# Kernel optimization log

Measured on AMD Instinct MI355X. Metric: run time of the kernel, lower is better.

Reference implementation:

```python
import jax, jax.numpy as jnp
import numpy as np

# Architecture constants (from init_kwargs / mamba_ssm Mamba2 defaults)
D_MODEL = 256
D_STATE = 64
D_CONV = 4
EXPAND = 2
HEADDIM = 64
D_INNER = EXPAND * D_MODEL          # 512
NHEADS = D_INNER // HEADDIM         # 8
CONV_DIM = D_INNER + 2 * D_STATE    # 640 (ngroups=1)
D_IN_PROJ = 2 * D_INNER + 2 * D_STATE + NHEADS  # 1160
NUM_LAYERS = 4
EPS = 1e-5


def _mamba2_block(h, ipw, cw, cb, dtb, alog, dpar, rmsw, opw):
    # h: (b, l, d_model)
    b, l, _ = h.shape
    zxbcdt = h @ ipw                                  # (b, l, D_IN_PROJ)
    z = zxbcdt[..., :D_INNER]
    xBC = zxbcdt[..., D_INNER:D_INNER + CONV_DIM]
    dt = zxbcdt[..., -NHEADS:]

    # causal depthwise conv1d over the sequence, then SiLU
    xBC = jnp.swapaxes(xBC, 1, 2)                     # (b, CONV_DIM, l)
    xBC = jax.lax.conv_general_dilated(
        xBC, cw[:, None, :], (1,), [(D_CONV - 1, 0)],
        feature_group_count=CONV_DIM)
    xBC = jax.nn.silu(xBC + cb[None, :, None])
    xBC = jnp.swapaxes(xBC, 1, 2)                     # (b, l, CONV_DIM)

    xh = xBC[..., :D_INNER].reshape(b, l, NHEADS, HEADDIM)
    Bm = xBC[..., D_INNER:D_INNER + D_STATE]          # (b, l, n)
    Cm = xBC[..., D_INNER + D_STATE:]                 # (b, l, n)

    dt = jax.nn.softplus(dt + dtb)                    # (b, l, h)
    A = -jnp.exp(alog)                                # (h,)

    def step(state, ins):
        # state: (b, h, p, n)
        x_t, dt_t, B_t, C_t = ins                     # (b,h,p),(b,h),(b,n),(b,n)
        dA = jnp.exp(dt_t * A)                        # (b, h)
        state = state * dA[:, :, None, None] + jnp.einsum('bh,bhp,bn->bhpn', dt_t, x_t, B_t)
        y = jnp.einsum('bhpn,bn->bhp', state, C_t)
        return state, y

    xs = (jnp.swapaxes(xh, 0, 1), jnp.swapaxes(dt, 0, 1),
          jnp.swapaxes(Bm, 0, 1), jnp.swapaxes(Cm, 0, 1))
    init = jnp.zeros((b, NHEADS, HEADDIM, D_STATE), h.dtype)
    _, ys = jax.lax.scan(step, init, xs)              # ys: (l, b, h, p)
    y = jnp.swapaxes(ys, 0, 1) + dpar[None, None, :, None] * xh
    y = y.reshape(b, l, D_INNER)

    # gated RMSNorm (norm(y * silu(z)) * weight), then out projection
    y = y * jax.nn.silu(z)
    y = y * jax.lax.rsqrt(jnp.mean(y * y, -1, keepdims=True) + EPS) * rmsw
    return y @ opw


def setup_inputs() -> dict:
    key = jax.random.key(0)
    ks = jax.random.split(key, 12)
    B, L, F = 16, 2048, 46
    inp = {
        'x': jax.random.normal(ks[0], (B, L, F), jnp.float32),
        'inp_w': jax.random.normal(ks[1], (F, D_MODEL), jnp.float32) * 0.1,
        'inp_b': jnp.zeros((D_MODEL,), jnp.float32),
        'in_proj_w': jax.random.normal(ks[2], (NUM_LAYERS, D_MODEL, D_IN_PROJ), jnp.float32) * 0.02,
        'conv_w': jax.random.normal(ks[3], (NUM_LAYERS, CONV_DIM, D_CONV), jnp.float32) * 0.2,
        'conv_b': jnp.zeros((NUM_LAYERS, CONV_DIM), jnp.float32),
        'dt_bias': jax.random.normal(ks[4], (NUM_LAYERS, NHEADS), jnp.float32) * 0.5,
        'A_log': jnp.log(jax.random.uniform(ks[5], (NUM_LAYERS, NHEADS), jnp.float32, 1.0, 16.0)),
        'D': jnp.ones((NUM_LAYERS, NHEADS), jnp.float32),
        'rms_w': jnp.ones((NUM_LAYERS, D_INNER), jnp.float32),
        'out_proj_w': jax.random.normal(ks[6], (NUM_LAYERS, D_INNER, D_MODEL), jnp.float32) * 0.02,
        'ln_w': jnp.ones((D_MODEL,), jnp.float32),
        'ln_b': jnp.zeros((D_MODEL,), jnp.float32),
        'dir_w': jax.random.normal(ks[7], (D_MODEL, 1), jnp.float32) * 0.05,
        'dir_b': jnp.zeros((1,), jnp.float32),
        'reg_w': jax.random.normal(ks[8], (D_MODEL, 3), jnp.float32) * 0.05,
        'reg_b': jnp.zeros((3,), jnp.float32),
    }
    return inp


def reference(x, inp_w, inp_b, in_proj_w, conv_w, conv_b, dt_bias, A_log, D,
              rms_w, out_proj_w, ln_w, ln_b, dir_w, dir_b, reg_w, reg_b):
    h = x @ inp_w + inp_b
    for i in range(NUM_LAYERS):
        h = h + _mamba2_block(h, in_proj_w[i], conv_w[i], conv_b[i], dt_bias[i],
                              A_log[i], D[i], rms_w[i], out_proj_w[i])
    mu = jnp.mean(h, -1, keepdims=True)
    var = jnp.mean((h - mu) ** 2, -1, keepdims=True)
    h = (h - mu) * jax.lax.rsqrt(var + EPS) * ln_w + ln_b
    h = jnp.mean(h, axis=1)                           # mean-pool over sequence
    # dropout is identity in eval mode
    dir_logits = h @ dir_w + dir_b
    reg_out = h @ reg_w + reg_b
    return (dir_logits, reg_out)
```

## Files before the change

kernel.cpp:

```cpp
#include <hip/hip_runtime.h>
#include <hip/hip_bf16.h>
#include <math.h>

typedef __hip_bfloat16 bf16;

#define B_ 16
#define L_ 2048
#define DM 256
#define DI 512
#define NH 8
#define HD 64
#define DS 64
#define CD 640
#define DIP 1160
#define XB 648
#define NP 1280
#define NL 4
#define Q_ 64
#define NCH 32
#define MROWS (B_*L_)
#define EPS_ 1e-5f
#define NIN 17
#define NSMALL 14
#define STGOFF 32
#define WIPT 28552
#define WOPT 683912
#define HMPOFF 946056
#define SLICEOFF 1011592
#define PERROW 2004

__device__ __forceinline__ float u2f(unsigned short u){ return __uint_as_float(((unsigned)u)<<16); }
__device__ __forceinline__ unsigned short f2bu(float f){ bf16 h = __float2bfloat16(f); return *(unsigned short*)&h; }
__device__ __forceinline__ float sigmoidf_(float x){ return 1.f/(1.f+__expf(-x)); }
__device__ __forceinline__ float siluf_(float x){ return x*sigmoidf_(x); }
__device__ __forceinline__ float softplusf_(float x){ return (x>20.f)? x : log1pf(__expf(x)); }

typedef __attribute__((ext_vector_type(8))) short short8v;
typedef __attribute__((ext_vector_type(4))) float float4v;
typedef __attribute__((ext_vector_type(8))) unsigned short ush8;

__device__ const int kN17[NIN] = {1507328,11776,256,1187840,10240,2560,32,32,32,2048,524288,256,256,256,1,768,3};
__device__ const int sIdx[NSMALL] = {1,2,4,5,6,7,8,9,11,12,13,14,15,16};
__device__ const int sNum[NSMALL] = {11776,256,10240,2560,32,32,32,2048,256,256,256,1,768,3};
__device__ const int sOff[NSMALL] = {0,11776,12032,22272,24832,24864,24896,24928,26976,27232,27488,27744,27748,28516};

struct PtrTab { const void* p[NIN]; };

__global__ __launch_bounds__(64) void k_sentinel(float* out, float v){
    int t = threadIdx.x;
    out[t] = (t==0) ? v : 0.f;
}

__global__ __launch_bounds__(256) void k_detect(PtrTab t, int* flags){
    int i = blockIdx.x;
    int n = kN17[i];
    int S = n < 4096 ? n : 4096;
    const unsigned short* u = (const unsigned short*)t.p[i];
    __shared__ int big, ze, zo, so;
    if (threadIdx.x == 0){ big=0; ze=0; zo=0; so=0; }
    __syncthreads();
    int lbig=0, lze=0, lzo=0, lso=0;
    for (int j=threadIdx.x; j<S; j+=256){
        unsigned short v = u[j];
        int e = (v>>7)&0xFF;
        if (e >= 131) lbig = 1;
        int isz = ((v & 0x7FFF) == 0) ? 1 : 0;
        if (j & 1){ lso++; lzo += isz; } else { lze += isz; }
    }
    if (lbig) atomicOr(&big, 1);
    atomicAdd(&ze, lze); atomicAdd(&zo, lzo); atomicAdd(&so, lso);
    __syncthreads();
    if (threadIdx.x == 0){
        int Se = S - so;
        flags[i] = (big || (so > 0 && 4*ze >= 3*Se && 4*zo <= so)) ? 1 : 0;
    }
}

__global__ __launch_bounds__(256) void k_stage(PtrTab t, const int* __restrict__ flags,
                                               float* __restrict__ stg){
    int a = blockIdx.y;
    int idx = sIdx[a];
    int n = sNum[a];
    float* dst = stg + sOff[a];
    const void* p = t.p[idx];
    if (flags[idx]){
        const float* s = (const float*)p;
        for (int j=blockIdx.x*256+threadIdx.x; j<n; j += gridDim.x*256) dst[j] = s[j];
    } else {
        const unsigned short* s = (const unsigned short*)p;
        for (int j=blockIdx.x*256+threadIdx.x; j<n; j += gridDim.x*256) dst[j] = u2f(s[j]);
    }
}

__global__ __launch_bounds__(256) void k_wip(const void* __restrict__ src,
                                             const int* __restrict__ flag,
                                             unsigned short* __restrict__ dst){
    int n = blockIdx.x, l = blockIdx.y, k = threadIdx.x;
    unsigned short b = 0;
    if (n < DIP){
        size_t si = ((size_t)l*DM + k)*DIP + n;
        if (flag[0]) b = f2bu(((const float*)src)[si]);
        else         b = ((const unsigned short*)src)[si];
    }
    dst[((size_t)l*NP + n)*DM + k] = b;
}

__global__ __launch_bounds__(256) void k_wop(const void* __restrict__ src,
                                             const int* __restrict__ flag,
                                             unsigned short* __restrict__ dst){
    int n = blockIdx.x, l = blockIdx.y;
    for (int k = threadIdx.x; k < DI; k += 256){
        size_t si = ((size_t)l*DI + k)*DM + n;
        unsigned short b;
        if (flag[0]) b = f2bu(((const float*)src)[si]);
        else         b = ((const unsigned short*)src)[si];
        dst[((size_t)l*DM + n)*DI + k] = b;
    }
}

__device__ __forceinline__ float blockSum256(float v, float* red){
    #pragma unroll
    for (int off=32; off>0; off>>=1) v += __shfl_down(v, off);
    if ((threadIdx.x & 63) == 0) red[threadIdx.x >> 6] = v;
    __syncthreads();
    float s = red[0] + red[1] + red[2] + red[3];
    __syncthreads();
    return s;
}

__global__ __launch_bounds__(256) void k_inproj(const void* __restrict__ x,
                                                const int* __restrict__ flags,
                                                size_t xoff,
                                                const float* __restrict__ w,
                                                const float* __restrict__ bias,
                                                float* __restrict__ h,
                                                unsigned short* __restrict__ hbf){
    __shared__ float xs[32*46];
    int row0 = blockIdx.x*32;
    int t = threadIdx.x;
    bool f32 = flags[0] != 0;
    for (int j = t; j < 32*46; j += 256){
        size_t gi = xoff + (size_t)row0*46 + j;
        xs[j] = f32 ? ((const float*)x)[gi] : u2f(((const unsigned short*)x)[gi]);
    }
    __syncthreads();
    float bv = bias[t];
    float acc[32];
    #pragma unroll
    for (int r=0;r<32;r++) acc[r] = bv;
    for (int k=0;k<46;k++){
        float wv = w[k*DM + t];
        #pragma unroll
        for (int r=0;r<32;r++) acc[r] += xs[r*46 + k]*wv;
    }
    #pragma unroll
    for (int r=0;r<32;r++){
        size_t o = (size_t)(row0 + r)*DM + t;
        h[o] = acc[r];
        hbf[o] = f2bu(acc[r]);
    }
}

template<int MODE>
__global__ __launch_bounds__(256, 4) void k_mgemm(const unsigned short* __restrict__ A,
                                                  const unsigned short* __restrict__ Bt,
                                                  float* __restrict__ O1,
                                                  unsigned short* __restrict__ O1b,
                                                  unsigned short* __restrict__ O2b,
                                                  unsigned short* __restrict__ O3,
                                                  int K){
    __shared__ __align__(16) char ldsraw[16896];
    unsigned short* As = (unsigned short*)ldsraw;
    unsigned short* Bs = (unsigned short*)(ldsraw + 5120);
    int tid = threadIdx.x;
    int wave = tid >> 6, lane = tid & 63, quad = lane >> 4, l15 = lane & 15;
    int p = blockIdx.y * gridDim.x + blockIdx.x;
    int nwg = gridDim.x * gridDim.y;
    int cpx = nwg >> 3;
    int logical = (p & 7) * cpx + (p >> 3);
    int by = logical / gridDim.x;
    int bx = logical - by * gridDim.x;
    int mbase = by*64, nbase = bx*128;
    int wm = (wave & 1)*32, wn = (wave >> 1)*64;
    float4v zero4 = {0.f,0.f,0.f,0.f};
    float4v acc[2][4];
    #pragma unroll
    for (int mi=0;mi<2;mi++)
        #pragma unroll
        for (int ni=0;ni<4;ni++) acc[mi][ni] = zero4;

    int rowA = tid >> 2, koffA = (tid & 3)*8;
    const unsigned short* Ap = A + (size_t)(mbase+rowA)*K + koffA;
    for (int k0 = 0; k0 < K; k0 += 32){
        *(uint4*)&As[rowA*40 + koffA] = *(const uint4*)&Ap[k0];
        #pragma unroll
        for (int i=0;i<2;i++){
            int c = tid + i*256;
            int row = c >> 2, koff = (c & 3)*8;
            *(uint4*)&Bs[row*40 + koff] = *(const uint4*)&Bt[(size_t)(nbase+row)*K + k0 + koff];
        }
        __syncthreads();
        short8v af[2], bfr[4];
        #pragma unroll
        for (int mi=0;mi<2;mi++) af[mi] = *(const short8v*)&As[(wm + mi*16 + l15)*40 + quad*8];
        #pragma unroll
        for (int ni=0;ni<4;ni++) bfr[ni] = *(const short8v*)&Bs[(wn + ni*16 + l15)*40 + quad*8];
        #pragma unroll
        for (int mi=0;mi<2;mi++)
            #pragma unroll
            for (int ni=0;ni<4;ni++)
                acc[mi][ni] = __builtin_amdgcn_mfma_f32_16x16x32_bf16(af[mi], bfr[ni], acc[mi][ni], 0, 0, 0);
        __syncthreads();
    }

    float* ep = (float*)ldsraw;
    int erow = tid >> 4;
    int ecc  = (tid & 15) * 8;
    #pragma unroll
    for (int half = 0; half < 2; ++half){
        if ((wave & 1) == half){
            #pragma unroll
            for (int mi=0;mi<2;mi++){
                #pragma unroll
                for (int ni=0;ni<4;ni++){
                    int col = wn + ni*16 + l15;
                    #pragma unroll
                    for (int reg=0;reg<4;reg++){
                        int r = mi*16 + quad*4 + reg;
                        ep[r*132 + col] = acc[mi][ni][reg];
                    }
                }
            }
        }
        __syncthreads();
        #pragma unroll
        for (int ps=0; ps<2; ps++){
            int r = ps*16 + erow;
            int growg = mbase + half*32 + r;
            int colg = nbase + ecc;
            float4 v0 = *(const float4*)&ep[r*132 + ecc + 0];
            float4 v1 = *(const float4*)&ep[r*132 + ecc + 4];
            if (MODE == 0){
                ush8 ob;
                ob[0]=f2bu(v0.x); ob[1]=f2bu(v0.y); ob[2]=f2bu(v0.z); ob[3]=f2bu(v0.w);
                ob[4]=f2bu(v1.x); ob[5]=f2bu(v1.y); ob[6]=f2bu(v1.z); ob[7]=f2bu(v1.w);
                if (colg + 8 <= DI){
                    *(ush8*)&O1b[(size_t)growg*DI + colg] = ob;
                } else if (colg >= DI && colg + 8 <= DIP){
                    *(ush8*)&O2b[(size_t)growg*XB + (colg - DI)] = ob;
                }
            } else {
                size_t ob1 = (size_t)growg*DM + colg;
                float4 h0 = *(const float4*)&O1[ob1];
                float4 h1 = *(const float4*)&O1[ob1+4];
                h0.x+=v0.x; h0.y+=v0.y; h0.z+=v0.z; h0.w+=v0.w;
                h1.x+=v1.x; h1.y+=v1.y; h1.z+=v1.z; h1.w+=v1.w;
                *(float4*)&O1[ob1] = h0;
                *(float4*)&O1[ob1+4] = h1;
                ush8 ob;
                ob[0]=f2bu(h0.x); ob[1]=f2bu(h0.y); ob[2]=f2bu(h0.z); ob[3]=f2bu(h0.w);
                ob[4]=f2bu(h1.x); ob[5]=f2bu(h1.y); ob[6]=f2bu(h1.z); ob[7]=f2bu(h1.w);
                *(ush8*)&O3[ob1] = ob;
            }
        }
        __syncthreads();
    }
}

__global__ __launch_bounds__(256) void k_conv(const unsigned short* __restrict__ xbb,
                                              const float* __restrict__ cw,
                                              const float* __restrict__ cb,
                                              unsigned short* __restrict__ cvb){
    int tid = threadIdx.x;
    int c0 = (blockIdx.x*16 + (tid & 15))*4;
    int r0 = blockIdx.y*64 + (tid >> 4);
    float wA[4], wB[4], wC[4], wD[4];
    {
        float4 t0 = *(const float4*)&cw[(size_t)(c0+0)*4];
        float4 t1 = *(const float4*)&cw[(size_t)(c0+1)*4];
        float4 t2 = *(const float4*)&cw[(size_t)(c0+2)*4];
        float4 t3 = *(const float4*)&cw[(size_t)(c0+3)*4];
        wA[0]=t0.x; wA[1]=t0.y; wA[2]=t0.z; wA[3]=t0.w;
        wB[0]=t1.x; wB[1]=t1.y; wB[2]=t1.z; wB[3]=t1.w;
        wC[0]=t2.x; wC[1]=t2.y; wC[2]=t2.z; wC[3]=t2.w;
        wD[0]=t3.x; wD[1]=t3.y; wD[2]=t3.z; wD[3]=t3.w;
    }
    float4 bb = *(const float4*)&cb[c0];
    #pragma unroll
    for (int i=0;i<4;i++){
        int r = r0 + i*16;
        int l = r & (L_-1);
        float a0=bb.x, a1=bb.y, a2=bb.z, a3=bb.w;
        #pragma unroll
        for (int j=0;j<4;j++){
            if (l-3+j >= 0){
                ushort4 uv = *(const ushort4*)&xbb[(size_t)(r-3+j)*XB + c0];
                a0 += u2f(uv.x)*wA[j];
                a1 += u2f(uv.y)*wB[j];
                a2 += u2f(uv.z)*wC[j];
                a3 += u2f(uv.w)*wD[j];
            }
        }
        ushort4 ov;
        ov.x = f2bu(siluf_(a0));
        ov.y = f2bu(siluf_(a1));
        ov.z = f2bu(siluf_(a2));
        ov.w = f2bu(siluf_(a3));
        *(ushort4*)&cvb[(size_t)r*CD + c0] = ov;
    }
}

__global__ __launch_bounds__(64) void k_dtcum(const unsigned short* __restrict__ xb,
                                              const float* __restrict__ dtb,
                                              const float* __restrict__ alog,
                                              float* __restrict__ dto,
                                              float* __restrict__ cumo){
    int kk = blockIdx.x, h = blockIdx.y, b = blockIdx.z;
    int t = threadIdx.x;
    int l = kk*Q_ + t;
    float raw = u2f(xb[(size_t)(b*L_ + l)*XB + CD + h]);
    float dtv = softplusf_(raw + dtb[h]);
    float A = -__expf(alog[h]);
    float s = dtv * A;
    #pragma unroll
    for (int off=1; off<64; off<<=1){
        float u = __shfl_up(s, off);
        if (t >= off) s += u;
    }
    int base = (b*NH + h)*L_ + l;
    dto[base] = dtv;
    cumo[base] = s;
}

__device__ __forceinline__ void grp_map(int p, int &kk, int &h, int &b){
    int c = p & 7, i = p >> 3;
    h = i & 7;
    int g = (i & ~7) | c;
    kk = g & (NCH-1);
    b = g >> 5;
}

__global__ __launch_bounds__(256) void k_passS(const unsigned short* __restrict__ cvb,
                                               const float* __restrict__ dt,
                                               const float* __restrict__ cum,
                                               float* __restrict__ S){
    __shared__ unsigned short Bw[64*72];
    __shared__ unsigned short Xt[64*72];
    __shared__ float sw[64];
    int kk, h, b;
    grp_map(blockIdx.x, kk, h, b);
    int tid = threadIdx.x;
    int bh = b*NH + h;
    int l0 = kk*Q_;
    if (tid < 64){
        int base = bh*L_ + l0;
        float c = cum[base + tid];
        float c63 = cum[base + 63];
        sw[tid] = dt[base + tid]*__expf(fminf(c63 - c, 0.f));
    }
    __syncthreads();
    int srow = tid >> 4, c0 = (tid & 15)*4;
    #pragma unroll
    for (int i=0;i<4;i++){
        int s = srow + i*16;
        size_t rb = ((size_t)(b*L_ + l0 + s))*CD;
        ushort4 bv = *(const ushort4*)&cvb[rb + DI + c0];
        ushort4 xv = *(const ushort4*)&cvb[rb + h*HD + c0];
        float w = sw[s];
        Bw[(c0+0)*72 + s] = f2bu(w*u2f(bv.x));
        Bw[(c0+1)*72 + s] = f2bu(w*u2f(bv.y));
        Bw[(c0+2)*72 + s] = f2bu(w*u2f(bv.z));
        Bw[(c0+3)*72 + s] = f2bu(w*u2f(bv.w));
        Xt[(c0+0)*72 + s] = xv.x;
        Xt[(c0+1)*72 + s] = xv.y;
        Xt[(c0+2)*72 + s] = xv.z;
        Xt[(c0+3)*72 + s] = xv.w;
    }
    __syncthreads();
    int wave = tid >> 6, lane = tid & 63, quad = lane >> 4, l15 = lane & 15;
    int wn = (wave & 1)*32, wp = (wave >> 1)*32;
    float4v zero4 = {0.f,0.f,0.f,0.f};
    float4v acc[2][2];
    #pragma unroll
    for (int mi=0;mi<2;mi++)
        #pragma unroll
        for (int ni=0;ni<2;ni++) acc[mi][ni] = zero4;
    #pragma unroll
    for (int k0=0;k0<64;k0+=32){
        short8v af[2], bfr[2];
        #pragma unroll
        for (int mi=0;mi<2;mi++) af[mi] = *(const short8v*)&Bw[(wn + mi*16 + l15)*72 + k0 + quad*8];
        #pragma unroll
        for (int ni=0;ni<2;ni++) bfr[ni] = *(const short8v*)&Xt[(wp + ni*16 + l15)*72 + k0 + quad*8];
        #pragma unroll
        for (int mi=0;mi<2;mi++)
            #pragma unroll
            for (int ni=0;ni<2;ni++)
                acc[mi][ni] = __builtin_amdgcn_mfma_f32_16x16x32_bf16(af[mi], bfr[ni], acc[mi][ni], 0, 0, 0);
    }
    size_t Sbase = ((size_t)bh*NCH + kk)*4096;
    #pragma unroll
    for (int mi=0;mi<2;mi++){
        #pragma unroll
        for (int ni=0;ni<2;ni++){
            int p = wp + ni*16 + l15;
            #pragma unroll
            for (int reg=0;reg<4;reg++){
                int n = wn + mi*16 + quad*4 + reg;
                S[Sbase + n*64 + p] = acc[mi][ni][reg];
            }
        }
    }
}

__global__ __launch_bounds__(256) void k_combine(const float* __restrict__ cum,
                                                 float* __restrict__ S){
    int h = blockIdx.x, b = blockIdx.y, z = blockIdx.z;
    int bh = b*NH + h;
    int tid = threadIdx.x;
    float4 st = make_float4(0.f,0.f,0.f,0.f);
    size_t base0 = ((size_t)bh*NCH)*4096 + (size_t)z*1024 + (size_t)tid*4;
    for (int k=0;k<NCH;k++){
        size_t base = base0 + (size_t)k*4096;
        float dk = __expf(fminf(cum[bh*L_ + k*Q_ + 63], 0.f));
        float4 a = *(const float4*)&S[base];
        *(float4*)&S[base] = st;
        st.x = a.x + dk*st.x;
        st.y = a.y + dk*st.y;
        st.z = a.z + dk*st.z;
        st.w = a.w + dk*st.w;
    }
}

__global__ __launch_bounds__(256) void k_finalize2(const unsigned short* __restrict__ cvb,
                                                   const float* __restrict__ dt,
                                                   const float* __restrict__ cum,
                                                   const float* __restrict__ Dp,
                                                   const float* __restrict__ S,
                                                   unsigned short* __restrict__ yB){
    __shared__ unsigned short Ct[64*72];
    __shared__ unsigned short Bs[64*72];
    __shared__ unsigned short Xt[64*72];
    __shared__ unsigned short St[64*72];
    __shared__ float sdt[64], scum[64];
    unsigned short* const Ml = &Bs[0];
    int kk, h, b;
    grp_map(blockIdx.x, kk, h, b);
    int tid = threadIdx.x;
    int bh = b*NH + h;
    int l0 = kk*Q_;
    if (tid < 64){
        int base = bh*L_ + l0;
        sdt[tid] = dt[base + tid];
        scum[tid] = cum[base + tid];
    }
    int rr = tid >> 4, c0 = (tid & 15)*4;
    size_t Sbase = ((size_t)bh*NCH + kk)*4096;
    #pragma unroll
    for (int i=0;i<4;i++){
        int r = rr + i*16;
        size_t rb = ((size_t)(b*L_ + l0 + r))*CD;
        *(ushort4*)&Ct[r*72 + c0] = *(const ushort4*)&cvb[rb + DI + DS + c0];
        *(ushort4*)&Bs[r*72 + c0] = *(const ushort4*)&cvb[rb + DI + c0];
        ushort4 xv = *(const ushort4*)&cvb[rb + h*HD + c0];
        Xt[(c0+0)*72 + r] = xv.x;
        Xt[(c0+1)*72 + r] = xv.y;
        Xt[(c0+2)*72 + r] = xv.z;
        Xt[(c0+3)*72 + r] = xv.w;
        float4 sv = *(const float4*)&S[Sbase + r*64 + c0];
        St[(c0+0)*72 + r] = f2bu(sv.x);
        St[(c0+1)*72 + r] = f2bu(sv.y);
        St[(c0+2)*72 + r] = f2bu(sv.z);
        St[(c0+3)*72 + r] = f2bu(sv.w);
    }
    __syncthreads();
    int wave = tid >> 6, lane = tid & 63, quad = lane >> 4, l15 = lane & 15;
    int wt2 = (wave & 1)*32, wc = (wave >> 1)*32;
    float4v zero4 = {0.f,0.f,0.f,0.f};
    {
        float4v acc[2][2];
        #pragma unroll
        for (int mi=0;mi<2;mi++)
            #pragma unroll
            for (int ni=0;ni<2;ni++) acc[mi][ni] = zero4;
        #pragma unroll
        for (int k0=0;k0<64;k0+=32){
            short8v af[2], bfr[2];
            #pragma unroll
            for (int mi=0;mi<2;mi++) af[mi] = *(const short8v*)&Ct[(wt2 + mi*16 + l15)*72 + k0 + quad*8];
            #pragma unroll
            for (int ni=0;ni<2;ni++) bfr[ni] = *(const short8v*)&Bs[(wc + ni*16 + l15)*72 + k0 + quad*8];
            #pragma unroll
            for (int mi=0;mi<2;mi++)
                #pragma unroll
                for (int ni=0;ni<2;ni++)
                    acc[mi][ni] = __builtin_amdgcn_mfma_f32_16x16x32_bf16(af[mi], bfr[ni], acc[mi][ni], 0, 0, 0);
        }
        __syncthreads();
        #pragma unroll
        for (int mi=0;mi<2;mi++){
            #pragma unroll
            for (int ni=0;ni<2;ni++){
                int s = wc + ni*16 + l15;
                #pragma unroll
                for (int reg=0;reg<4;reg++){
                    int t = wt2 + mi*16 + quad*4 + reg;
                    float m = (s <= t) ? acc[mi][ni][reg]*sdt[s]*__expf(fminf(scum[t]-scum[s], 0.f)) : 0.f;
                    Ml[t*72 + s] = f2bu(m);
                }
            }
        }
    }
    __syncthreads();
    {
        float4v a1[2][2], a2[2][2];
        #pragma unroll
        for (int mi=0;mi<2;mi++)
            #pragma unroll
            for (int ni=0;ni<2;ni++){ a1[mi][ni] = zero4; a2[mi][ni] = zero4; }
        #pragma unroll
        for (int k0=0;k0<64;k0+=32){
            short8v mf[2], cf[2], xf[2], sf[2];
            #pragma unroll
            for (int mi=0;mi<2;mi++){
                mf[mi] = *(const short8v*)&Ml[(wt2 + mi*16 + l15)*72 + k0 + quad*8];
                cf[mi] = *(const short8v*)&Ct[(wt2 + mi*16 + l15)*72 + k0 + quad*8];
            }
            #pragma unroll
            for (int ni=0;ni<2;ni++){
                xf[ni] = *(const short8v*)&Xt[(wc + ni*16 + l15)*72 + k0 + quad*8];
                sf[ni] = *(const short8v*)&St[(wc + ni*16 + l15)*72 + k0 + quad*8];
            }
            #pragma unroll
            for (int mi=0;mi<2;mi++)
                #pragma unroll
                for (int ni=0;ni<2;ni++){
                    a1[mi][ni] = __builtin_amdgcn_mfma_f32_16x16x32_bf16(mf[mi], xf[ni], a1[mi][ni], 0, 0, 0);
                    a2[mi][ni] = __builtin_amdgcn_mfma_f32_16x16x32_bf16(cf[mi], sf[ni], a2[mi][ni], 0, 0, 0);
                }
        }
        float Dh = Dp[h];
        #pragma unroll
        for (int mi=0;mi<2;mi++){
            #pragma unroll
            for (int ni=0;ni<2;ni++){
                int p = wc + ni*16 + l15;
                #pragma unroll
                for (int reg=0;reg<4;reg++){
                    int t = wt2 + mi*16 + quad*4 + reg;
                    float e = __expf(fminf(scum[t], 0.f));
                    float xval = u2f(Xt[p*72 + t]);
                    yB[(size_t)(b*L_ + l0 + t)*DI + h*HD + p] =
                        f2bu(a1[mi][ni][reg] + e*a2[mi][ni][reg] + Dh*xval);
                }
            }
        }
    }
}

__global__ __launch_bounds__(256) void k_gaterms(const unsigned short* __restrict__ z,
                                                 const float* __restrict__ rw,
                                                 const unsigned short* __restrict__ yB,
                                                 unsigned short* __restrict__ ybf){
    __shared__ float red[4];
    int row = blockIdx.x;
    int tid = threadIdx.x;
    float g[2]; float ss = 0.f;
    #pragma unroll
    for (int r=0;r<2;r++){
        int d = tid + r*256;
        float zv = u2f(z[(size_t)row*DI + d]);
        float yv = u2f(yB[(size_t)row*DI + d]);
        float gv = yv * siluf_(zv);
        g[r] = gv;
        ss += gv*gv;
    }
    float tot = blockSum256(ss, red);
    float rinv = rsqrtf(tot*(1.f/512.f) + EPS_);
    #pragma unroll
    for (int r=0;r<2;r++){
        int d = tid + r*256;
        ybf[(size_t)row*DI + d] = f2bu(g[r]*rinv*rw[d]);
    }
}

__global__ __launch_bounds__(256) void k_ln(const float* __restrict__ h,
                                            const float* __restrict__ lw,
                                            const float* __restrict__ lb,
                                            float* __restrict__ out){
    __shared__ float red[4];
    int row = blockIdx.x;
    int tid = threadIdx.x;
    float v = h[(size_t)row*DM + tid];
    float mu = blockSum256(v, red)*(1.f/256.f);
    float d = v - mu;
    float var = blockSum256(d*d, red)*(1.f/256.f);
    out[(size_t)row*DM + tid] = d*rsqrtf(var + EPS_)*lw[tid] + lb[tid];
}

__global__ __launch_bounds__(256) void k_meanl(const float* __restrict__ ln,
                                               float* __restrict__ hmp,
                                               int b0){
    int g = blockIdx.x, bl = blockIdx.y;
    int tid = threadIdx.x;
    float s = 0.f;
    for (int i=0;i<128;i++){
        int l = g*128 + i;
        s += ln[(size_t)(bl*L_ + l)*DM + tid];
    }
    hmp[((size_t)(b0+bl)*16 + g)*DM + tid] = s*(1.f/2048.f);
}

__global__ __launch_bounds__(256) void k_heads(const float* __restrict__ hmp,
                                               const float* __restrict__ dw,
                                               const float* __restrict__ db,
                                               const float* __restrict__ rw,
                                               const float* __restrict__ rb,
                                               float* __restrict__ out){
    __shared__ float red[4];
    int b = blockIdx.x;
    int tid = threadIdx.x;
    float hv = 0.f;
    #pragma unroll
    for (int g=0; g<16; g++) hv += hmp[((size_t)b*16 + g)*DM + tid];
    float s0 = hv*dw[tid];
    float s1 = hv*rw[tid*3+0];
    float s2 = hv*rw[tid*3+1];
    float s3 = hv*rw[tid*3+2];
    s0 = blockSum256(s0, red);
    s1 = blockSum256(s1, red);
    s2 = blockSum256(s2, red);
    s3 = blockSum256(s3, red);
    if (tid == 0){
        out[b] = s0 + db[0];
        out[16 + b*3 + 0] = s1 + rb[0];
        out[16 + b*3 + 1] = s2 + rb[1];
        out[16 + b*3 + 2] = s3 + rb[2];
    }
}

extern "C" void kernel_launch(void* const* d_in, const int* in_sizes, int n_in,
                              void* d_out, int out_size, void* d_ws, size_t ws_size,
                              hipStream_t stream){
    static const int expSizes[NIN] = {1507328,11776,256,1187840,10240,2560,32,32,32,2048,524288,256,256,256,1,768,3};
    float* out = (float*)d_out;

    if (n_in != NIN){
        k_sentinel<<<1,64,0,stream>>>(out, 9.0e6f);
        return;
    }
    for (int i=0;i<NIN;i++){
        if (in_sizes[i] != expSizes[i]){
            k_sentinel<<<1,64,0,stream>>>(out, (float)(i+1)*1.0e5f);
            return;
        }
    }
    size_t need16 = ((size_t)SLICEOFF + 2048ull*PERROW)*4ull;
    if (ws_size < need16){
        float mb = (float)(ws_size >> 20);
        k_sentinel<<<1,64,0,stream>>>(out, 2.0e7f + mb*131072.f);
        return;
    }

    float* ws = (float*)d_ws;
    int* flags = (int*)d_ws;
    float* stg = ws + STGOFF;
    unsigned short* ipwT = (unsigned short*)(ws + WIPT);
    unsigned short* opwT = (unsigned short*)(ws + WOPT);
    float* hmp = ws + HMPOFF;

    PtrTab pt;
    for (int i=0;i<NIN;i++) pt.p[i] = d_in[i];

    k_detect<<<NIN, 256, 0, stream>>>(pt, flags);
    k_stage<<<dim3(8, NSMALL), 256, 0, stream>>>(pt, flags, stg);
    k_wip<<<dim3(NP, NL), 256, 0, stream>>>(d_in[3], flags+3, ipwT);
    k_wop<<<dim3(DM, NL), 256, 0, stream>>>(d_in[10], flags+10, opwT);

    const float* inp_w = stg + 0;
    const float* inp_b = stg + 11776;
    const float* cw    = stg + 12032;
    const float* cb    = stg + 22272;
    const float* dtb   = stg + 24832;
    const float* alog  = stg + 24864;
    const float* Dp    = stg + 24896;
    const float* rmsw  = stg + 24928;
    const float* lnw   = stg + 26976;
    const float* lnb   = stg + 27232;
    const float* dw    = stg + 27488;
    const float* db    = stg + 27744;
    const float* rw    = stg + 27748;
    const float* rb    = stg + 28516;

    int nsl = 1;
    while (((size_t)SLICEOFF + ((size_t)MROWS/nsl)*PERROW)*4ull > ws_size) nsl <<= 1;
    const size_t R = (size_t)MROWS / nsl;
    const int SB = B_ / nsl;

    float* base = ws + SLICEOFF;
    float* hbuf = base;
    unsigned short* hbf  = (unsigned short*)(base + R*256);
    unsigned short* zb   = (unsigned short*)(base + R*384);
    unsigned short* xbb  = (unsigned short*)(base + R*640);
    unsigned short* ybB  = (unsigned short*)(base + R*640);
    unsigned short* cvb  = (unsigned short*)(base + R*964);
    unsigned short* ybf  = (unsigned short*)(base + R*964);
    float* S   = base + R*1284;
    float* dt  = base + R*1796;
    float* cum = base + R*1804;

    for (int sl=0; sl<nsl; sl++){
        k_inproj<<<(int)(R/32), 256, 0, stream>>>(d_in[0], flags, (size_t)sl*R*46, inp_w, inp_b, hbuf, hbf);
        for (int li=0; li<NL; li++){
            const float* cwl = cw + li*CD*4;
            const float* cbl = cb + li*CD;
            k_mgemm<0><<<dim3(NP/128, R/64), 256, 0, stream>>>(
                hbf, ipwT + (size_t)li*NP*DM, hbuf, zb, xbb, ybf, DM);
            k_conv<<<dim3(10, (int)(R/64)), 256, 0, stream>>>(xbb, cwl, cbl, cvb);
            k_dtcum<<<dim3(NCH,NH,SB), 64, 0, stream>>>(xbb, dtb + li*NH, alog + li*NH, dt, cum);
            k_passS<<<NCH*NH*SB, 256, 0, stream>>>(cvb, dt, cum, S);
            k_combine<<<dim3(NH,SB,4), 256, 0, stream>>>(cum, S);
            k_finalize2<<<NCH*NH*SB, 256, 0, stream>>>(cvb, dt, cum, Dp + li*NH, S, ybB);
            k_gaterms<<<(int)R, 256, 0, stream>>>(zb, rmsw + li*DI, ybB, ybf);
            k_mgemm<1><<<dim3(DM/128, R/64), 256, 0, stream>>>(
                ybf, opwT + (size_t)li*DM*DI, hbuf, zb, xbb, hbf, DI);
        }
        k_ln<<<(int)R, 256, 0, stream>>>(hbuf, lnw, lnb, S);
        k_meanl<<<dim3(16,SB), 256, 0, stream>>>(S, hmp, sl*SB);
    }
    k_heads<<<B_, 256, 0, stream>>>(hmp, dw, db, rw, rb, out);
}
```

Before: 1.041 ms.

## Fuse dt cumsum into conv, store chunk states as bf16, fuse layernorm with mean-pool

Folds the dt softplus/cumsum kernel into an extra block column of the conv kernel, which removes one launch per layer. The combine pass now writes the chunk-prefix states as bf16 in place, so finalize reads half the bytes. The final layernorm and sequence mean-pool become one kernel that accumulates with atomics, which needs a zeroing kernel first. The GEMM epilogue LDS row stride is padded from 132 to 140 to reduce bank conflicts. The in-place bf16 aliasing of S relies on a per-block syncthreads ordering, and the atomics make the summation order nondeterministic.

Measured after the change: 998.6 us. 1.04x faster.

```diff
diff --git a/kernel.cpp b/kernel.cpp
--- a/kernel.cpp
+++ b/kernel.cpp
@@ -118,6 +118,10 @@
     }
 }
 
+__global__ __launch_bounds__(256) void k_zerohmp(float* __restrict__ hmp){
+    hmp[(size_t)blockIdx.x*256 + threadIdx.x] = 0.f;
+}
+
 __device__ __forceinline__ float blockSum256(float v, float* red){
     #pragma unroll
     for (int off=32; off>0; off>>=1) v += __shfl_down(v, off);
@@ -169,7 +173,7 @@
                                                   unsigned short* __restrict__ O2b,
                                                   unsigned short* __restrict__ O3,
                                                   int K){
-    __shared__ __align__(16) char ldsraw[16896];
+    __shared__ __align__(16) char ldsraw[17920];
     unsigned short* As = (unsigned short*)ldsraw;
     unsigned short* Bs = (unsigned short*)(ldsraw + 5120);
     int tid = threadIdx.x;
@@ -227,7 +231,7 @@
                     #pragma unroll
                     for (int reg=0;reg<4;reg++){
                         int r = mi*16 + quad*4 + reg;
-                        ep[r*132 + col] = acc[mi][ni][reg];
+                        ep[r*140 + col] = acc[mi][ni][reg];
                     }
                 }
             }
@@ -238,8 +242,8 @@
             int r = ps*16 + erow;
             int growg = mbase + half*32 + r;
             int colg = nbase + ecc;
-            float4 v0 = *(const float4*)&ep[r*132 + ecc + 0];
-            float4 v1 = *(const float4*)&ep[r*132 + ecc + 4];
+            float4 v0 = *(const float4*)&ep[r*140 + ecc + 0];
+            float4 v1 = *(const float4*)&ep[r*140 + ecc + 4];
             if (MODE == 0){
                 ush8 ob;
                 ob[0]=f2bu(v0.x); ob[1]=f2bu(v0.y); ob[2]=f2bu(v0.z); ob[3]=f2bu(v0.w);
@@ -270,8 +274,35 @@
 __global__ __launch_bounds__(256) void k_conv(const unsigned short* __restrict__ xbb,
                                               const float* __restrict__ cw,
                                               const float* __restrict__ cb,
+                                              const float* __restrict__ dtb,
+                                              const float* __restrict__ alog,
+                                              float* __restrict__ dto,
+                                              float* __restrict__ cumo,
                                               unsigned short* __restrict__ cvb){
     int tid = threadIdx.x;
+    if (blockIdx.x == 10){
+        int r0 = blockIdx.y*64;
+        int b = r0 >> 11;
+        int l0 = r0 & (L_-1);
+        int wave = tid >> 6, t = tid & 63;
+        #pragma unroll
+        for (int hh = 0; hh < 2; hh++){
+            int h = wave + hh*4;
+            float raw = u2f(xbb[(size_t)(r0 + t)*XB + CD + h]);
+            float dtv = softplusf_(raw + dtb[h]);
+            float A = -__expf(alog[h]);
+            float s = dtv * A;
+            #pragma unroll
+            for (int off=1; off<64; off<<=1){
+                float u = __shfl_up(s, off);
+                if (t >= off) s += u;
+            }
+            int base = (b*NH + h)*L_ + l0 + t;
+            dto[base] = dtv;
+            cumo[base] = s;
+        }
+        return;
+    }
     int c0 = (blockIdx.x*16 + (tid & 15))*4;
     int r0 = blockIdx.y*64 + (tid >> 4);
     float wA[4], wB[4], wC[4], wD[4];
@@ -308,28 +339,6 @@
         ov.w = f2bu(siluf_(a3));
         *(ushort4*)&cvb[(size_t)r*CD + c0] = ov;
     }
-}
-
-__global__ __launch_bounds__(64) void k_dtcum(const unsigned short* __restrict__ xb,
-                                              const float* __restrict__ dtb,
-                                              const float* __restrict__ alog,
-                                              float* __restrict__ dto,
-                                              float* __restrict__ cumo){
-    int kk = blockIdx.x, h = blockIdx.y, b = blockIdx.z;
-    int t = threadIdx.x;
-    int l = kk*Q_ + t;
-    float raw = u2f(xb[(size_t)(b*L_ + l)*XB + CD + h]);
-    float dtv = softplusf_(raw + dtb[h]);
-    float A = -__expf(alog[h]);
-    float s = dtv * A;
-    #pragma unroll
-    for (int off=1; off<64; off<<=1){
-        float u = __shfl_up(s, off);
-        if (t >= off) s += u;
-    }
-    int base = (b*NH + h)*L_ + l;
-    dto[base] = dtv;
-    cumo[base] = s;
 }
 
 __device__ __forceinline__ void grp_map(int p, int &kk, int &h, int &b){
@@ -414,17 +423,22 @@
 }
 
 __global__ __launch_bounds__(256) void k_combine(const float* __restrict__ cum,
-                                                 float* __restrict__ S){
+                                                 float* __restrict__ S,
+                                                 unsigned short* __restrict__ Sb){
     int h = blockIdx.x, b = blockIdx.y, z = blockIdx.z;
     int bh = b*NH + h;
     int tid = threadIdx.x;
     float4 st = make_float4(0.f,0.f,0.f,0.f);
-    size_t base0 = ((size_t)bh*NCH)*4096 + (size_t)z*1024 + (size_t)tid*4;
+    size_t chunk0 = ((size_t)bh*NCH)*4096;
+    int qoff = z*1024 + tid*4;
     for (int k=0;k<NCH;k++){
-        size_t base = base0 + (size_t)k*4096;
+        size_t cb = chunk0 + (size_t)k*4096;
         float dk = __expf(fminf(cum[bh*L_ + k*Q_ + 63], 0.f));
-        float4 a = *(const float4*)&S[base];
-        *(float4*)&S[base] = st;
+        float4 a = *(const float4*)&S[cb + qoff];
+        __syncthreads();
+        ushort4 pb;
+        pb.x = f2bu(st.x); pb.y = f2bu(st.y); pb.z = f2bu(st.z); pb.w = f2bu(st.w);
+        *(ushort4*)&Sb[2*(cb + (size_t)z*1024) + tid*4] = pb;
         st.x = a.x + dk*st.x;
         st.y = a.y + dk*st.y;
         st.z = a.z + dk*st.z;
@@ -436,7 +450,7 @@
                                                    const float* __restrict__ dt,
                                                    const float* __restrict__ cum,
                                                    const float* __restrict__ Dp,
-                                                   const float* __restrict__ S,
+                                                   const unsigned short* __restrict__ Sb,
                                                    unsigned short* __restrict__ yB){
     __shared__ unsigned short Ct[64*72];
     __shared__ unsigned short Bs[64*72];
@@ -467,11 +481,14 @@
         Xt[(c0+1)*72 + r] = xv.y;
         Xt[(c0+2)*72 + r] = xv.z;
         Xt[(c0+3)*72 + r] = xv.w;
-        float4 sv = *(const float4*)&S[Sbase + r*64 + c0];
-        St[(c0+0)*72 + r] = f2bu(sv.x);
-        St[(c0+1)*72 + r] = f2bu(sv.y);
-        St[(c0+2)*72 + r] = f2bu(sv.z);
-        St[(c0+3)*72 + r] = f2bu(sv.w);
+        int wfull = r*64 + c0;
+        int zq = wfull >> 10;
+        size_t u = 2*(Sbase + ((size_t)zq<<10)) + (wfull & 1023);
+        ushort4 sv = *(const ushort4*)&Sb[u];
+        St[(c0+0)*72 + r] = sv.x;
+        St[(c0+1)*72 + r] = sv.y;
+        St[(c0+2)*72 + r] = sv.z;
+        St[(c0+3)*72 + r] = sv.w;
     }
     __syncthreads();
     int wave = tid >> 6, lane = tid & 63, quad = lane >> 4, l15 = lane & 15;
@@ -584,31 +601,27 @@
     }
 }
 
-__global__ __launch_bounds__(256) void k_ln(const float* __restrict__ h,
-                                            const float* __restrict__ lw,
-                                            const float* __restrict__ lb,
-                                            float* __restrict__ out){
+__global__ __launch_bounds__(256) void k_lnmean(const float* __restrict__ h,
+                                                const float* __restrict__ lw,
+                                                const float* __restrict__ lb,
+                                                float* __restrict__ hmp,
+                                                int b0){
     __shared__ float red[4];
-    int row = blockIdx.x;
     int tid = threadIdx.x;
-    float v = h[(size_t)row*DM + tid];
-    float mu = blockSum256(v, red)*(1.f/256.f);
-    float d = v - mu;
-    float var = blockSum256(d*d, red)*(1.f/256.f);
-    out[(size_t)row*DM + tid] = d*rsqrtf(var + EPS_)*lw[tid] + lb[tid];
-}
-
-__global__ __launch_bounds__(256) void k_meanl(const float* __restrict__ ln,
-                                               float* __restrict__ hmp,
-                                               int b0){
-    int g = blockIdx.x, bl = blockIdx.y;
-    int tid = threadIdx.x;
-    float s = 0.f;
-    for (int i=0;i<128;i++){
-        int l = g*128 + i;
-        s += ln[(size_t)(bl*L_ + l)*DM + tid];
-    }
-    hmp[((size_t)(b0+bl)*16 + g)*DM + tid] = s*(1.f/2048.f);
+    int r0 = blockIdx.x*8;
+    int bl = r0 >> 11;
+    int g = (r0 & (L_-1)) >> 7;
+    float lwv = lw[tid], lbv = lb[tid];
+    float accv = 0.f;
+    for (int i=0;i<8;i++){
+        int row = r0 + i;
+        float v = h[(size_t)row*DM + tid];
+        float mu = blockSum256(v, red)*(1.f/256.f);
+        float d = v - mu;
+        float var = blockSum256(d*d, red)*(1.f/256.f);
+        accv += d*rsqrtf(var + EPS_)*lwv + lbv;
+    }
+    atomicAdd(&hmp[((size_t)(b0+bl)*16 + g)*DM + tid], accv*(1.f/2048.f));
 }
 
 __global__ __launch_bounds__(256) void k_heads(const float* __restrict__ hmp,
@@ -676,6 +689,7 @@
     k_stage<<<dim3(8, NSMALL), 256, 0, stream>>>(pt, flags, stg);
     k_wip<<<dim3(NP, NL), 256, 0, stream>>>(d_in[3], flags+3, ipwT);
     k_wop<<<dim3(DM, NL), 256, 0, stream>>>(d_in[10], flags+10, opwT);
+    k_zerohmp<<<B_*16*DM/256, 256, 0, stream>>>(hmp);
 
     const float* inp_w = stg + 0;
     const float* inp_b = stg + 11776;
@@ -716,17 +730,17 @@
             const float* cbl = cb + li*CD;
             k_mgemm<0><<<dim3(NP/128, R/64), 256, 0, stream>>>(
                 hbf, ipwT + (size_t)li*NP*DM, hbuf, zb, xbb, ybf, DM);
-            k_conv<<<dim3(10, (int)(R/64)), 256, 0, stream>>>(xbb, cwl, cbl, cvb);
-            k_dtcum<<<dim3(NCH,NH,SB), 64, 0, stream>>>(xbb, dtb + li*NH, alog + li*NH, dt, cum);
+            k_conv<<<dim3(11, (int)(R/64)), 256, 0, stream>>>(
+                xbb, cwl, cbl, dtb + li*NH, alog + li*NH, dt, cum, cvb);
             k_passS<<<NCH*NH*SB, 256, 0, stream>>>(cvb, dt, cum, S);
-            k_combine<<<dim3(NH,SB,4), 256, 0, stream>>>(cum, S);
-            k_finalize2<<<NCH*NH*SB, 256, 0, stream>>>(cvb, dt, cum, Dp + li*NH, S, ybB);
+            k_combine<<<dim3(NH,SB,4), 256, 0, stream>>>(cum, S, (unsigned short*)S);
+            k_finalize2<<<NCH*NH*SB, 256, 0, stream>>>(cvb, dt, cum, Dp + li*NH,
+                (const unsigned short*)S, ybB);
             k_gaterms<<<(int)R, 256, 0, stream>>>(zb, rmsw + li*DI, ybB, ybf);
             k_mgemm<1><<<dim3(DM/128, R/64), 256, 0, stream>>>(
                 ybf, opwT + (size_t)li*DM*DI, hbuf, zb, xbb, hbf, DI);
         }
-        k_ln<<<(int)R, 256, 0, stream>>>(hbuf, lnw, lnb, S);
-        k_meanl<<<dim3(16,SB), 256, 0, stream>>>(S, hmp, sl*SB);
+        k_lnmean<<<(int)(R/8), 256, 0, stream>>>(hbuf, lnw, lnb, hmp, sl*SB);
     }
     k_heads<<<B_, 256, 0, stream>>>(hmp, dw, db, rw, rb, out);
 }
```
